# Kernel tuning notes

Measured on AMD Instinct MI355X. Metric: run time of the kernel, lower is better.

The kernel has to match this reference:

```python
import jax, jax.numpy as jnp
import numpy as np

F4_E2M1_MAX = 6.0
F8E4M3_MAX = 448.0
E4M3_EPS = 0.015625  # torch.finfo(float8_e4m3fn).tiny = 2**-6
BLOCK = 16
KE2M1 = jnp.array([0.0, 0.5, 1.0, 1.5, 2.0, 3.0, 4.0, 6.0], dtype=jnp.float32)


def round_to_e4m3(x):
    # emulate cast to float8_e4m3fn and back (round-to-nearest-even)
    return x.astype(jnp.float8_e4m3fn).astype(jnp.float32)


def fp4_121_positive(x):
    step1 = jnp.round(2.0 * x) / 2.0   # subnormal-ish region [0,2): step 0.5
    step2 = jnp.round(x)               # [2,4): step 1
    step3 = 2.0 * jnp.round(x / 2.0)   # [4,6]: step 2
    return jnp.where(x < 2.0, step1, jnp.where(x < 4.0, step2, step3))


def cast_to_fp4(x):
    return jnp.sign(x) * fp4_121_positive(jnp.abs(x))


def unpack_fp4_from_uint8(a, m, n):
    # a: int-typed tensor holding byte values in [0,256); two fp4 codes per byte
    high = (a.reshape(-1) >> 4) & 0xF
    low = a.reshape(-1) & 0xF
    combined = jnp.stack((low, high), axis=1).reshape(m, n)  # interleave low,high
    signs = (combined & 8) != 0
    abs_idx = combined & 7
    return KE2M1[abs_idx] * jnp.where(signs, -1.0, 1.0)


def dequant_nvfp4_packed(data_lp, out_scales, per_tensor_scale):
    m, half_n = data_lp.shape
    n = half_n * 2
    data_hp = unpack_fp4_from_uint8(data_lp, m, n)           # [m, n] float32
    scale_fp = out_scales / per_tensor_scale                  # [m, n/16]
    data_hp = data_hp.reshape(m, -1, BLOCK) * scale_fp.reshape(m, -1, 1)
    return data_hp.reshape(m, n)


def qdq_nvfp4(x):
    m, n = x.shape
    tensor_amax = jnp.max(jnp.abs(x))
    pts = jnp.clip(tensor_amax / F8E4M3_MAX, E4M3_EPS, F8E4M3_MAX)  # per-tensor scale
    xb = x.reshape(m, -1, BLOCK)
    block_scale = jnp.max(jnp.abs(xb), axis=-1) / F4_E2M1_MAX       # [m, n/16]
    scaled_bs = round_to_e4m3(jnp.clip(block_scale / pts, E4M3_EPS, F8E4M3_MAX))
    total_scale = pts * scaled_bs                                   # [m, n/16]
    data_scaled = jnp.clip(xb / total_scale[..., None], -F4_E2M1_MAX, F4_E2M1_MAX)
    data_lp = cast_to_fp4(data_scaled)                              # unpacked fp4 values
    # dequant: out_scales / (1/pts) == scaled_bs * pts == total_scale
    return (data_lp * total_scale[..., None]).reshape(m, n)


def setup_inputs() -> dict:
    key = jax.random.key(0)
    k1, k2, k3 = jax.random.split(key, 3)
    M, K, N = 16384, 2048, 2048  # tokens, in_features, out_features
    x = jax.random.normal(k1, (M, K), dtype=jnp.float32)
    weight_packed = jax.random.randint(k2, (N, K // 2), 0, 256, dtype=jnp.int32)
    # fp8-representable positive block scales
    weight_scale = round_to_e4m3(jax.random.uniform(k3, (N, K // 16), dtype=jnp.float32,
                                                    minval=0.05, maxval=1.0))
    weight_global_scale = jnp.ones((1,), dtype=jnp.float32)
    return {"x": x, "weight_packed": weight_packed,
            "weight_scale": weight_scale, "weight_global_scale": weight_global_scale}


def reference(x, weight_packed, weight_scale, weight_global_scale):
    hp_weight = dequant_nvfp4_packed(weight_packed, weight_scale, weight_global_scale)
    x_dq = qdq_nvfp4(x)
    return x_dq @ hp_weight.T
```

## Files before the change

kernel.cpp:

```cpp
#include <hip/hip_runtime.h>

typedef unsigned short u16;
typedef unsigned int u32;
typedef __attribute__((ext_vector_type(8))) short short8;
typedef __attribute__((ext_vector_type(4))) float floatx4;

static constexpr int M = 16384, N = 2048, K = 2048;


__device__ inline u16 f32_to_bf16(float x) {
    u32 u = __float_as_uint(x);
    u += 0x7FFFu + ((u >> 16) & 1u);
    return (u16)(u >> 16);
}

__device__ inline float e4m3_rne(float x) {
    u32 u = __float_as_uint(x);
    u += 0x7FFFFu + ((u >> 20) & 1u);
    u &= 0xFFF00000u;
    return __uint_as_float(u);
}

__device__ inline float fp4_dec(u32 c) {
    u32 e = (c >> 1) & 3u;
    float m = (float)(c & 1u);
    float v = e ? (2.0f + m) * (float)(1u << e) * 0.25f : 0.5f * m;
    return (c & 8u) ? -v : v;
}

__device__ inline float fp4_round_mag(float a) {
    if (a < 2.0f) return rintf(2.0f * a) * 0.5f;
    if (a < 4.0f) return rintf(a);
    return 2.0f * rintf(a * 0.5f);
}

__device__ inline float pts_from_amax(float amax) {
    return fminf(fmaxf(amax / 448.0f, 0.015625f), 448.0f);
}


__global__ void amax_part(const float4* __restrict__ x, float* __restrict__ part, int n4) {
    int idx = blockIdx.x * blockDim.x + threadIdx.x;
    int stride = gridDim.x * blockDim.x;
    float m = 0.0f;
    for (int i = idx; i < n4; i += stride) {
        float4 v = x[i];
        m = fmaxf(m, fmaxf(fmaxf(fabsf(v.x), fabsf(v.y)), fmaxf(fabsf(v.z), fabsf(v.w))));
    }
#pragma unroll
    for (int off = 32; off > 0; off >>= 1)
        m = fmaxf(m, __shfl_down(m, off));
    __shared__ float sm[4];
    if ((threadIdx.x & 63) == 0) sm[threadIdx.x >> 6] = m;
    __syncthreads();
    if (threadIdx.x == 0)
        part[blockIdx.x] = fmaxf(fmaxf(sm[0], sm[1]), fmaxf(sm[2], sm[3]));
}


__global__ void amax_fin(const float* __restrict__ part, u32* __restrict__ out) {
    int t = threadIdx.x;
    float m = fmaxf(part[t], part[t + 1024]);
#pragma unroll
    for (int off = 32; off > 0; off >>= 1)
        m = fmaxf(m, __shfl_down(m, off));
    __shared__ float sm[16];
    if ((t & 63) == 0) sm[t >> 6] = m;
    __syncthreads();
    if (t < 16) {
        m = sm[t];
#pragma unroll
        for (int off = 8; off > 0; off >>= 1)
            m = fmaxf(m, __shfl_down(m, off));
        if (t == 0) *out = __float_as_uint(m);
    }
}


static constexpr int QB = (M * K / 4) / 256;
static constexpr int DB = (N * (K / 2)) / 256;

__global__ void prep(const float4* __restrict__ x, uint2* __restrict__ aq,
                     const u32* __restrict__ amax_bits,
                     const int* __restrict__ wp, const float* __restrict__ wsc,
                     const float* __restrict__ wgs, u16* __restrict__ wq) {
    if (blockIdx.x < QB) {
        int idx = blockIdx.x * blockDim.x + threadIdx.x;
        float4 v = x[idx];

        float bm = fmaxf(fmaxf(fabsf(v.x), fabsf(v.y)), fmaxf(fabsf(v.z), fabsf(v.w)));
        bm = fmaxf(bm, __shfl_xor(bm, 1));
        bm = fmaxf(bm, __shfl_xor(bm, 2));

        float pts = pts_from_amax(__uint_as_float(*amax_bits));
        float bs = bm / 6.0f;
        float sbs = e4m3_rne(fminf(fmaxf(bs / pts, 0.015625f), 448.0f));
        float ts = pts * sbs;

        float vf[4] = {v.x, v.y, v.z, v.w};
        u16 o[4];
#pragma unroll
        for (int i = 0; i < 4; i++) {
            float s = vf[i] / ts;
            s = fminf(fmaxf(s, -6.0f), 6.0f);
            float lp = copysignf(fp4_round_mag(fabsf(s)), s);
            o[i] = f32_to_bf16(lp * sbs);
        }
        aq[idx] = *(const uint2*)o;
    } else {
        int idx = (blockIdx.x - QB) * blockDim.x + threadIdx.x;
        constexpr int Khalf = K / 2;
        int n = idx >> 10;
        int kb = idx & (Khalf - 1);
        u32 byte = (u32)wp[idx] & 0xFFu;
        float scale = wsc[(size_t)n * (K / 16) + (kb >> 3)] / wgs[0];
        float lo = fp4_dec(byte & 0xFu) * scale;
        float hi = fp4_dec((byte >> 4) & 0xFu) * scale;
        u32 out = (u32)f32_to_bf16(lo) | ((u32)f32_to_bf16(hi) << 16);
        ((u32*)wq)[idx] = out;
    }
}


#define GLDS(g, l)                                                              \
    __builtin_amdgcn_global_load_lds(                                           \
        (const __attribute__((address_space(1))) unsigned int*)(g),             \
        (__attribute__((address_space(3))) unsigned int*)(l), 16, 0, 0)

__global__ __launch_bounds__(256, 3) void gemm_bt(
    const u16* __restrict__ A, const u16* __restrict__ B,
    float* __restrict__ C, const u32* __restrict__ amax_bits)
{
    __shared__ u16 lA[2][128 * 32];
    __shared__ u16 lB[2][128 * 32];

    const int tid = threadIdx.x;
    const int w = tid >> 6, lane = tid & 63;

    const int id = blockIdx.x;
    const int xcd = id & 7;
    const int local = id >> 3;
    const int bm = xcd * 16 + (local >> 4);
    const int bn = local & 15;

    const int wm = w >> 1, wn = w & 1;
    const int r = lane & 15, q = lane >> 4;

    floatx4 acc[4][4] = {};

    const int srow = lane >> 2;
    const int scol = (lane & 3) * 8;
    const u16* gA0 = A + (size_t)(bm * 128 + w * 32 + srow) * K + scol;
    const u16* gA1 = gA0 + (size_t)16 * K;
    const u16* gB0 = B + (size_t)(bn * 128 + w * 32 + srow) * K + scol;
    const u16* gB1 = gB0 + (size_t)16 * K;
    u16* dA[2][2], * dB[2][2];
#pragma unroll
    for (int h = 0; h < 2; h++) {
        dA[h][0] = &lA[h][(w * 32) * 32];
        dA[h][1] = &lA[h][(w * 32 + 16) * 32];
        dB[h][0] = &lB[h][(w * 32) * 32];
        dB[h][1] = &lB[h][(w * 32 + 16) * 32];
    }

    for (int kt = 0; kt < K; kt += 64) {
        GLDS(gA0 + kt,      dA[0][0]);
        GLDS(gA1 + kt,      dA[0][1]);
        GLDS(gA0 + kt + 32, dA[1][0]);
        GLDS(gA1 + kt + 32, dA[1][1]);
        GLDS(gB0 + kt,      dB[0][0]);
        GLDS(gB1 + kt,      dB[0][1]);
        GLDS(gB0 + kt + 32, dB[1][0]);
        GLDS(gB1 + kt + 32, dB[1][1]);
        __syncthreads();

#pragma unroll
        for (int h = 0; h < 2; h++) {
            short8 af[4], bf[4];
#pragma unroll
            for (int i = 0; i < 4; i++)
                af[i] = *(const short8*)&lA[h][(wm * 64 + i * 16 + r) * 32 + q * 8];
#pragma unroll
            for (int j = 0; j < 4; j++)
                bf[j] = *(const short8*)&lB[h][(wn * 64 + j * 16 + r) * 32 + q * 8];

#pragma unroll
            for (int i = 0; i < 4; i++)
#pragma unroll
                for (int j = 0; j < 4; j++)
                    acc[i][j] = __builtin_amdgcn_mfma_f32_16x16x32_bf16(
                        af[i], bf[j], acc[i][j], 0, 0, 0);
        }

        __syncthreads();
    }

    float pts = pts_from_amax(__uint_as_float(*amax_bits));

    float* Cb = C + (size_t)(bm * 128 + wm * 64 + q * 4) * N + bn * 128 + wn * 64 + r;
#pragma unroll
    for (int i = 0; i < 4; i++)
#pragma unroll
        for (int j = 0; j < 4; j++)
#pragma unroll
            for (int t = 0; t < 4; t++)
                Cb[(size_t)(i * 16 + t) * N + j * 16] = pts * acc[i][j][t];
}


extern "C" void kernel_launch(void* const* d_in, const int* in_sizes, int n_in,
                              void* d_out, int out_size, void* d_ws, size_t ws_size,
                              hipStream_t stream) {
    const float* x   = (const float*)d_in[0];
    const int*   wp  = (const int*)d_in[1];
    const float* wsc = (const float*)d_in[2];
    const float* wgs = (const float*)d_in[3];
    float* out = (float*)d_out;

    u32*   amax_ws = (u32*)d_ws;
    float* part    = (float*)((char*)d_ws + 64);
    u16*   aq      = (u16*)((char*)d_ws + 16384);
    u16*   wq      = aq + (size_t)M * K;

    amax_part<<<2048, 256, 0, stream>>>((const float4*)x, part, M * K / 4);
    amax_fin<<<1, 1024, 0, stream>>>(part, amax_ws);
    prep<<<QB + DB, 256, 0, stream>>>((const float4*)x, (uint2*)aq, amax_ws,
                                      wp, wsc, wgs, wq);
    gemm_bt<<<(M / 128) * (N / 128), 256, 0, stream>>>(aq, wq, out, amax_ws);
}
```

Measured before the change: 406.0 us.

## Enlarge GEMM tiles to 256x256 and add 4-stage async LDS pipeline

The bf16 GEMM moves from 128x128 tiles with 256 threads to 256x256 tiles with 512 threads. Each wave now computes a 128x64 sub-tile, which raises data reuse per LDS load. The per-iteration double `__syncthreads` loop is replaced by a 4-slot ring of `global_load_lds` stages. Explicit `vmcnt` waits and a single barrier per step let three stages be in flight while the current slab is computed. In exchange, LDS use grows to 128KB per block, which limits occupancy to about one block per CU, and each thread holds more accumulator registers.

```diff
diff --git a/kernel.cpp b/kernel.cpp
--- a/kernel.cpp
+++ b/kernel.cpp
@@ -127,12 +127,29 @@
         (const __attribute__((address_space(1))) unsigned int*)(g),             \
         (__attribute__((address_space(3))) unsigned int*)(l), 16, 0, 0)
 
-__global__ __launch_bounds__(256, 3) void gemm_bt(
+__device__ inline void compute_slab(const u16* __restrict__ sA,
+                                    const u16* __restrict__ sB,
+                                    floatx4 acc[8][4]) {
+    short8 af[8], bf[4];
+#pragma unroll
+    for (int i = 0; i < 8; i++) af[i] = *(const short8*)(sA + i * 512);
+#pragma unroll
+    for (int j = 0; j < 4; j++) bf[j] = *(const short8*)(sB + j * 512);
+#pragma unroll
+    for (int i = 0; i < 8; i++)
+#pragma unroll
+        for (int j = 0; j < 4; j++)
+            acc[i][j] = __builtin_amdgcn_mfma_f32_16x16x32_bf16(
+                af[i], bf[j], acc[i][j], 0, 0, 0);
+}
+
+__global__ __launch_bounds__(512, 2) void gemm_bt(
     const u16* __restrict__ A, const u16* __restrict__ B,
     float* __restrict__ C, const u32* __restrict__ amax_bits)
 {
-    __shared__ u16 lA[2][128 * 32];
-    __shared__ u16 lB[2][128 * 32];
+    __shared__ u16 lA[4][256 * 32];
+    __shared__ u16 lB[4][256 * 32];
+    constexpr int SLOT = 256 * 32;
 
     const int tid = threadIdx.x;
     const int w = tid >> 6, lane = tid & 63;
@@ -140,66 +157,68 @@
     const int id = blockIdx.x;
     const int xcd = id & 7;
     const int local = id >> 3;
-    const int bm = xcd * 16 + (local >> 4);
-    const int bn = local & 15;
-
-    const int wm = w >> 1, wn = w & 1;
-    const int r = lane & 15, q = lane >> 4;
-
-    floatx4 acc[4][4] = {};
+    const int bm = xcd * 8 + (local >> 3);
+    const int bn = local & 7;
+
+    const int wm = w >> 2, wn = w & 3;
+    const int r16 = lane & 15, q = lane >> 4;
+
+    floatx4 acc[8][4] = {};
 
     const int srow = lane >> 2;
-    const int scol = (lane & 3) * 8;
-    const u16* gA0 = A + (size_t)(bm * 128 + w * 32 + srow) * K + scol;
-    const u16* gA1 = gA0 + (size_t)16 * K;
-    const u16* gB0 = B + (size_t)(bn * 128 + w * 32 + srow) * K + scol;
-    const u16* gB1 = gB0 + (size_t)16 * K;
-    u16* dA[2][2], * dB[2][2];
-#pragma unroll
-    for (int h = 0; h < 2; h++) {
-        dA[h][0] = &lA[h][(w * 32) * 32];
-        dA[h][1] = &lA[h][(w * 32 + 16) * 32];
-        dB[h][0] = &lB[h][(w * 32) * 32];
-        dB[h][1] = &lB[h][(w * 32 + 16) * 32];
-    }
-
-    for (int kt = 0; kt < K; kt += 64) {
-        GLDS(gA0 + kt,      dA[0][0]);
-        GLDS(gA1 + kt,      dA[0][1]);
-        GLDS(gA0 + kt + 32, dA[1][0]);
-        GLDS(gA1 + kt + 32, dA[1][1]);
-        GLDS(gB0 + kt,      dB[0][0]);
-        GLDS(gB1 + kt,      dB[0][1]);
-        GLDS(gB0 + kt + 32, dB[1][0]);
-        GLDS(gB1 + kt + 32, dB[1][1]);
-        __syncthreads();
-
-#pragma unroll
-        for (int h = 0; h < 2; h++) {
-            short8 af[4], bf[4];
-#pragma unroll
-            for (int i = 0; i < 4; i++)
-                af[i] = *(const short8*)&lA[h][(wm * 64 + i * 16 + r) * 32 + q * 8];
-#pragma unroll
-            for (int j = 0; j < 4; j++)
-                bf[j] = *(const short8*)&lB[h][(wn * 64 + j * 16 + r) * 32 + q * 8];
-
-#pragma unroll
-            for (int i = 0; i < 4; i++)
-#pragma unroll
-                for (int j = 0; j < 4; j++)
-                    acc[i][j] = __builtin_amdgcn_mfma_f32_16x16x32_bf16(
-                        af[i], bf[j], acc[i][j], 0, 0, 0);
-        }
-
-        __syncthreads();
-    }
+    const int sq8 = (lane & 3) * 8;
+    const u16* gA0 = A + (size_t)(bm * 256 + (w * 2 + 0) * 16 + srow) * K + sq8;
+    const u16* gA1 = A + (size_t)(bm * 256 + (w * 2 + 1) * 16 + srow) * K + sq8;
+    const u16* gB0 = B + (size_t)(bn * 256 + (w * 2 + 0) * 16 + srow) * K + sq8;
+    const u16* gB1 = B + (size_t)(bn * 256 + (w * 2 + 1) * 16 + srow) * K + sq8;
+    u16* dA0 = &lA[0][(w * 2 + 0) * 512];
+    u16* dA1 = &lA[0][(w * 2 + 1) * 512];
+    u16* dB0 = &lB[0][(w * 2 + 0) * 512];
+    u16* dB1 = &lB[0][(w * 2 + 1) * 512];
+
+#define STAGE(u) do {                                                          \
+        const int _s = (u) & 3; const int _kt = (u) * 32;                      \
+        GLDS(gA0 + _kt, dA0 + _s * SLOT);                                      \
+        GLDS(gA1 + _kt, dA1 + _s * SLOT);                                      \
+        GLDS(gB0 + _kt, dB0 + _s * SLOT);                                      \
+        GLDS(gB1 + _kt, dB1 + _s * SLOT);                                      \
+    } while (0)
+
+    const u16* sAb = &lA[0][(wm * 128 + r16) * 32 + q * 8];
+    const u16* sBb = &lB[0][(wn * 64 + r16) * 32 + q * 8];
+
+    constexpr int NT = K / 32;
+
+    STAGE(0); STAGE(1); STAGE(2);
+
+#pragma unroll 1
+    for (int t = 0; t < NT - 3; ++t) {
+        asm volatile("s_waitcnt vmcnt(8)" ::: "memory");
+        __builtin_amdgcn_s_barrier();
+        __builtin_amdgcn_sched_barrier(0);
+        STAGE(t + 3);
+        const int s = t & 3;
+        compute_slab(sAb + s * SLOT, sBb + s * SLOT, acc);
+    }
+    asm volatile("s_waitcnt vmcnt(8)" ::: "memory");
+    __builtin_amdgcn_s_barrier();
+    __builtin_amdgcn_sched_barrier(0);
+    compute_slab(sAb + ((NT - 3) & 3) * SLOT, sBb + ((NT - 3) & 3) * SLOT, acc);
+    asm volatile("s_waitcnt vmcnt(4)" ::: "memory");
+    __builtin_amdgcn_s_barrier();
+    __builtin_amdgcn_sched_barrier(0);
+    compute_slab(sAb + ((NT - 2) & 3) * SLOT, sBb + ((NT - 2) & 3) * SLOT, acc);
+    asm volatile("s_waitcnt vmcnt(0)" ::: "memory");
+    __builtin_amdgcn_s_barrier();
+    __builtin_amdgcn_sched_barrier(0);
+    compute_slab(sAb + ((NT - 1) & 3) * SLOT, sBb + ((NT - 1) & 3) * SLOT, acc);
 
     float pts = pts_from_amax(__uint_as_float(*amax_bits));
 
-    float* Cb = C + (size_t)(bm * 128 + wm * 64 + q * 4) * N + bn * 128 + wn * 64 + r;
-#pragma unroll
-    for (int i = 0; i < 4; i++)
+    float* Cb = C + (size_t)(bm * 256 + wm * 128 + q * 4) * N
+                  + bn * 256 + wn * 64 + r16;
+#pragma unroll
+    for (int i = 0; i < 8; i++)
 #pragma unroll
         for (int j = 0; j < 4; j++)
 #pragma unroll
@@ -226,5 +245,5 @@
     amax_fin<<<1, 1024, 0, stream>>>(part, amax_ws);
     prep<<<QB + DB, 256, 0, stream>>>((const float4*)x, (uint2*)aq, amax_ws,
                                       wp, wsc, wgs, wq);
-    gemm_bt<<<(M / 128) * (N / 128), 256, 0, stream>>>(aq, wq, out, amax_ws);
-}
+    gemm_bt<<<(M / 256) * (N / 256), 512, 0, stream>>>(aq, wq, out, amax_ws);
+}
```

New measurement: 458.3 us. 12.9% more time.
